# Kernel tuning notes

Measured on AMD Instinct MI355X. Metric: run time of the kernel, lower is better.

## Reference

```python
import jax, jax.numpy as jnp
import numpy as np

N_HEADS = 16
LN_EPS = 1e-5


def setup_inputs() -> dict:
    key = jax.random.key(0)
    ks = jax.random.split(key, 7)
    B, N, DIN, DCOND, NF = 2, 512, 1024, 128, 8
    return {
        "x": jax.random.normal(ks[0], (B, N, DIN), jnp.float32),
        "code": jax.random.normal(ks[1], (DCOND, NF), jnp.float32),
        "w_c": jax.random.normal(ks[2], (DIN, DCOND), jnp.float32) * 0.02,
        "W": jax.random.normal(ks[3], (3 * DIN, DIN), jnp.float32) * 0.02,
        "b": jax.random.normal(ks[4], (3 * DIN,), jnp.float32) * 0.02,
        "gamma": jnp.ones((DIN,), jnp.float32),
        "beta": jnp.zeros((DIN,), jnp.float32),
    }


def _layernorm(h, gamma, beta):
    mu = jnp.mean(h, axis=-1, keepdims=True)
    var = jnp.var(h, axis=-1, keepdims=True)
    return (h - mu) * jax.lax.rsqrt(var + LN_EPS) * gamma + beta


def reference(x, code, w_c, W, b, gamma, beta):
    B, N, din = x.shape
    nf = code.shape[1]
    H = N_HEADS
    hd = din // H
    scale = hd ** (-0.5)

    # ModLin2D: condition codes -> (nf, din), layernormed
    cond = _layernorm((w_c @ code).T, gamma, beta)            # (nf, din)
    # FiLM-style broadcasted multiply: (B, nf, N, din)
    modx = x[:, None, :, :] * cond[None, :, None, :]
    # projection to qkv: (B, nf, N, 3*din)
    qkv = jnp.einsum('bfnd,ed->bfne', modx, W) + b

    # split channel dim as (3, H, hd); torch view(3,H,hd,B,nf,N) on
    # channel-first layout == reshape (..., 3, H, hd) here
    qkv = qkv.reshape(B, nf, N, 3, H, hd)
    qkv = jnp.transpose(qkv, (3, 0, 4, 1, 2, 5))              # (3, B, H, nf, N, hd)
    q, k = qkv[0], qkv[1]

    scores = jnp.einsum('bhfnd,bhfmd->bhfnm', q, k) * scale   # (B, H, nf, N, N)
    attn = jax.nn.softmax(scores, axis=-1)
    # original torch code returns attn.size(); we return attn (the computed tensor)
    return attn
```

## Files before the change

kernel.cpp:

```cpp
#include <hip/hip_runtime.h>
#include <hip/hip_bf16.h>
#include <math.h>

#define NB    2
#define NSEQ  512
#define DIN   1024
#define DCOND 128
#define NF    8
#define NH    16
#define HD    64
constexpr float LN_EPS = 1e-5f;

#define WS_COND 0
#define WS_AHI  32768
#define WS_ALO  16809984
#define WS_BHI  33587200
#define WS_BLO  37781504
#define WS_QB   41975808
#define WS_KB   75530240

using bf16x8 = __attribute__((ext_vector_type(8))) short;
using f32x4  = __attribute__((ext_vector_type(4))) float;

__device__ __forceinline__ unsigned short f2bf(float x) {
    unsigned int u = __float_as_uint(x);
    unsigned int r = (u + 0x7fffu + ((u >> 16) & 1u)) >> 16;
    return (unsigned short)r;
}
__device__ __forceinline__ float bf2f(unsigned short h) {
    return __uint_as_float(((unsigned int)h) << 16);
}

__device__ __forceinline__ void gload16(const void* g, void* l) {
    __builtin_amdgcn_global_load_lds(
        (__attribute__((address_space(1))) void*)(const_cast<void*>(g)),
        (__attribute__((address_space(3))) void*)l, 16, 0, 0);
}

struct BF2 { bf16x8 hi, lo; };
__device__ __forceinline__ BF2 split8(float4 a, float4 b) {
    float v[8] = {a.x, a.y, a.z, a.w, b.x, b.y, b.z, b.w};
    BF2 r;
#pragma unroll
    for (int i = 0; i < 8; ++i) {
        unsigned u  = __float_as_uint(v[i]);
        unsigned uh = u & 0xffff0000u;
        r.hi[i] = (short)(u >> 16);
        float l = v[i] - __uint_as_float(uh);
        r.lo[i] = (short)(__float_as_uint(l) >> 16);
    }
    return r;
}

__global__ __launch_bounds__(256)
void cond_kernel(const float* __restrict__ w_c, const float* __restrict__ code,
                 const float* __restrict__ gamma, const float* __restrict__ beta,
                 float* __restrict__ cond)
{
    __shared__ float sc[DCOND];
    __shared__ float rs[256], rs2[256];
    const int f = blockIdx.x;
    const int t = threadIdx.x;

    if (t < DCOND) sc[t] = code[t * NF + f];
    __syncthreads();

    float hv[4];
    float s = 0.f, s2 = 0.f;
#pragma unroll
    for (int r = 0; r < 4; ++r) {
        const int d = r * 256 + t;
        const float* row = w_c + (size_t)d * DCOND;
        float acc = 0.f;
#pragma unroll 8
        for (int c = 0; c < DCOND; c += 4) {
            float4 wv = *(const float4*)(row + c);
            float4 cv = *(const float4*)(sc + c);
            acc += wv.x * cv.x + wv.y * cv.y + wv.z * cv.z + wv.w * cv.w;
        }
        hv[r] = acc; s += acc; s2 += acc * acc;
    }
    rs[t] = s; rs2[t] = s2;
    __syncthreads();
    for (int off = 128; off > 0; off >>= 1) {
        if (t < off) { rs[t] += rs[t + off]; rs2[t] += rs2[t + off]; }
        __syncthreads();
    }
    const float mu  = rs[0] * (1.f / DIN);
    const float var = rs2[0] * (1.f / DIN) - mu * mu;
    const float rstd = rsqrtf(var + LN_EPS);
#pragma unroll
    for (int r = 0; r < 4; ++r) {
        const int d = r * 256 + t;
        cond[f * DIN + d] = (hv[r] - mu) * rstd * gamma[d] + beta[d];
    }
}

__global__ __launch_bounds__(256)
void split_x_kernel(const float* __restrict__ x, const float* __restrict__ cond,
                    short* __restrict__ Ahi, short* __restrict__ Alo)
{
    const unsigned idx = blockIdx.x * 256 + threadIdx.x;
    const int d  = (idx & 127) * 8;
    const int n  = (idx >> 7) & 511;
    const int bf = idx >> 16;
    const int b  = bf >> 3, f = bf & 7;

    const float* xs = x + ((size_t)b * NSEQ + n) * DIN + d;
    const float* cs = cond + f * DIN + d;
    float4 x0 = *(const float4*)xs, x1 = *(const float4*)(xs + 4);
    float4 c0 = *(const float4*)cs, c1 = *(const float4*)(cs + 4);

    float m[8] = { x0.x*c0.x, x0.y*c0.y, x0.z*c0.z, x0.w*c0.w,
                   x1.x*c1.x, x1.y*c1.y, x1.z*c1.z, x1.w*c1.w };
    bf16x8 hi, lo;
#pragma unroll
    for (int i = 0; i < 8; ++i) {
        unsigned short h = f2bf(m[i]);
        hi[i] = (short)h;
        lo[i] = (short)f2bf(m[i] - bf2f(h));
    }
    *(bf16x8*)(Ahi + (size_t)idx * 8) = hi;
    *(bf16x8*)(Alo + (size_t)idx * 8) = lo;
}

__global__ __launch_bounds__(256)
void split_w_kernel(const float* __restrict__ W,
                    short* __restrict__ Bhi, short* __restrict__ Blo)
{
    const unsigned idx = blockIdx.x * 256 + threadIdx.x;
    const float* ws = W + (size_t)idx * 8;
    float4 w0 = *(const float4*)ws, w1 = *(const float4*)(ws + 4);
    float m[8] = { w0.x, w0.y, w0.z, w0.w, w1.x, w1.y, w1.z, w1.w };
    bf16x8 hi, lo;
#pragma unroll
    for (int i = 0; i < 8; ++i) {
        unsigned short h = f2bf(m[i]);
        hi[i] = (short)h;
        lo[i] = (short)f2bf(m[i] - bf2f(h));
    }
    *(bf16x8*)(Bhi + (size_t)idx * 8) = hi;
    *(bf16x8*)(Blo + (size_t)idx * 8) = lo;
}

__global__ __launch_bounds__(256, 2)
void proj_mfma_kernel(const short* __restrict__ Ahi_g, const short* __restrict__ Alo_g,
                      const short* __restrict__ Bhi_g, const short* __restrict__ Blo_g,
                      const float* __restrict__ bias,
                      float* __restrict__ Qb, float* __restrict__ Kb)
{
    __shared__ short sAhi[128 * 32];
    __shared__ short sAlo[128 * 32];
    __shared__ short sBhi[128 * 32];
    __shared__ short sBlo[128 * 32];

    const int bf   = blockIdx.z;
    const int n0   = blockIdx.y * 128;
    const int bcol = blockIdx.x * 128;
    const int t    = threadIdx.x;
    const int w    = t >> 6, lane = t & 63;
    const int wr   = w >> 1, wc = w & 1;

    const int rl = lane >> 2;
    const int sl = (lane & 3) ^ ((lane >> 3) & 3);
    const size_t aoff = ((size_t)bf * NSEQ + n0 + 32 * w + rl) * DIN + sl * 8;
    const size_t boff = ((size_t)(bcol + 32 * w + rl)) * DIN + sl * 8;
    const short* gAh = Ahi_g + aoff;
    const short* gAl = Alo_g + aoff;
    const short* gBh = Bhi_g + boff;
    const short* gBl = Blo_g + boff;
    short* dAh = sAhi + 1024 * w;
    short* dAl = sAlo + 1024 * w;
    short* dBh = sBhi + 1024 * w;
    short* dBl = sBlo + 1024 * w;

    int offA[4], offB[4];
    const int g = lane >> 4;
#pragma unroll
    for (int fi = 0; fi < 4; ++fi) {
        int r  = wr * 64 + fi * 16 + (lane & 15);
        offA[fi] = r * 32 + ((g ^ ((r >> 1) & 3)) * 8);
        int rb = wc * 64 + fi * 16 + (lane & 15);
        offB[fi] = rb * 32 + ((g ^ ((rb >> 1) & 3)) * 8);
    }

    f32x4 acc[4][4];
#pragma unroll
    for (int i = 0; i < 4; ++i)
#pragma unroll
        for (int j = 0; j < 4; ++j) acc[i][j] = (f32x4){0.f, 0.f, 0.f, 0.f};

    for (int kb = 0; kb < DIN; kb += 32) {
        __syncthreads();
        gload16(gAh + kb, dAh);  gload16(gAh + kb + 16 * DIN, dAh + 512);
        gload16(gAl + kb, dAl);  gload16(gAl + kb + 16 * DIN, dAl + 512);
        gload16(gBh + kb, dBh);  gload16(gBh + kb + 16 * DIN, dBh + 512);
        gload16(gBl + kb, dBl);  gload16(gBl + kb + 16 * DIN, dBl + 512);
        __syncthreads();

        bf16x8 Ah[4], Al[4], Bh[4], Bl[4];
#pragma unroll
        for (int fi = 0; fi < 4; ++fi) {
            Ah[fi] = *(const bf16x8*)(sAhi + offA[fi]);
            Al[fi] = *(const bf16x8*)(sAlo + offA[fi]);
            Bh[fi] = *(const bf16x8*)(sBhi + offB[fi]);
            Bl[fi] = *(const bf16x8*)(sBlo + offB[fi]);
        }
#pragma unroll
        for (int i = 0; i < 4; ++i)
#pragma unroll
            for (int j = 0; j < 4; ++j) {
                acc[i][j] = __builtin_amdgcn_mfma_f32_16x16x32_bf16(Ah[i], Bh[j], acc[i][j], 0, 0, 0);
                acc[i][j] = __builtin_amdgcn_mfma_f32_16x16x32_bf16(Ah[i], Bl[j], acc[i][j], 0, 0, 0);
                acc[i][j] = __builtin_amdgcn_mfma_f32_16x16x32_bf16(Al[i], Bh[j], acc[i][j], 0, 0, 0);
            }
    }

#pragma unroll
    for (int j = 0; j < 4; ++j) {
        const int e = bcol + wc * 64 + j * 16 + (lane & 15);
        const float bv = bias[e];
        const int ek = e & 1023;
        float* dst = ((e < DIN) ? Qb : Kb)
                   + ((size_t)(bf * NH + (ek >> 6)) * NSEQ) * HD + (ek & 63);
#pragma unroll
        for (int i = 0; i < 4; ++i) {
            const int rbase = n0 + wr * 64 + i * 16 + (lane >> 4) * 4;
            f32x4 v = acc[i][j];
#pragma unroll
            for (int rg = 0; rg < 4; ++rg)
                dst[(size_t)(rbase + rg) * HD] = v[rg] + bv;
        }
    }
}

__global__ __launch_bounds__(256, 2)
void scores_mfma_kernel(const float* __restrict__ Qb, const float* __restrict__ Kb,
                        float* __restrict__ out)
{
    __shared__ float Kl_lds[128 * 64];

    const int bfh = blockIdx.y;
    const int rt  = blockIdx.x;
    const int t = threadIdx.x, w = t >> 6, lane = t & 63;
    const int g = lane >> 4, c16 = lane & 15;

    const float* Qp = Qb + ((size_t)bfh * NSEQ + rt * 64 + 16 * w + c16) * HD;
    BF2 qf[2];
#pragma unroll
    for (int ks = 0; ks < 2; ++ks) {
        float4 a = *(const float4*)(Qp + 32 * ks + 8 * g);
        float4 b = *(const float4*)(Qp + 32 * ks + 8 * g + 4);
        qf[ks] = split8(a, b);
    }

    const float* Kp = Kb + (size_t)bfh * NSEQ * HD;
    const int swz = (lane & 7) << 4;

    f32x4 acc[32];
#pragma unroll
    for (int i = 0; i < 32; ++i) acc[i] = (f32x4){0.f, 0.f, 0.f, 0.f};

#pragma unroll
    for (int c = 0; c < 4; ++c) {
        __syncthreads();
#pragma unroll
        for (int i = 0; i < 8; ++i) {
            const int row = 32 * w + 4 * i + g;
            const int slot = c16 ^ (row & 7);
            gload16(Kp + ((size_t)(c * 128 + row)) * HD + slot * 4,
                    Kl_lds + (32 * w + 4 * i) * HD);
        }
        __syncthreads();

#pragma unroll
        for (int mtl = 0; mtl < 8; ++mtl) {
            const int row = 16 * mtl + c16;
            const char* rbase = (const char*)Kl_lds + row * 256;
#pragma unroll
            for (int ks = 0; ks < 2; ++ks) {
                const int o = 128 * ks + 32 * g;
                float4 a = *(const float4*)(rbase + ((o)      ^ swz));
                float4 b = *(const float4*)(rbase + ((o + 16) ^ swz));
                BF2 kf = split8(a, b);
                f32x4 d = acc[c * 8 + mtl];
                d = __builtin_amdgcn_mfma_f32_16x16x32_bf16(kf.hi, qf[ks].hi, d, 0, 0, 0);
                d = __builtin_amdgcn_mfma_f32_16x16x32_bf16(kf.hi, qf[ks].lo, d, 0, 0, 0);
                d = __builtin_amdgcn_mfma_f32_16x16x32_bf16(kf.lo, qf[ks].hi, d, 0, 0, 0);
                acc[c * 8 + mtl] = d;
            }
        }
    }

    float m = -1e30f;
#pragma unroll
    for (int i = 0; i < 32; ++i)
#pragma unroll
        for (int r = 0; r < 4; ++r) m = fmaxf(m, acc[i][r]);
    m = fmaxf(m, __shfl_xor(m, 16));
    m = fmaxf(m, __shfl_xor(m, 32));

    float s = 0.f;
#pragma unroll
    for (int i = 0; i < 32; ++i)
#pragma unroll
        for (int r = 0; r < 4; ++r) {
            float e = __expf((acc[i][r] - m) * 0.125f);
            acc[i][r] = e;
            s += e;
        }
    s += __shfl_xor(s, 16);
    s += __shfl_xor(s, 32);
    const float inv = 1.f / s;

    const int b = bfh >> 7, f = (bfh >> 4) & 7, h = bfh & 15;
    const int n = rt * 64 + 16 * w + c16;
    float* rowp = out + ((((size_t)(b * NH + h)) * NF + f) * NSEQ + n) * NSEQ;
#pragma unroll
    for (int i = 0; i < 32; ++i) {
        f32x4 v = acc[i] * inv;
        *(f32x4*)(rowp + 16 * i + 4 * g) = v;
    }
}

extern "C" void kernel_launch(void* const* d_in, const int* in_sizes, int n_in,
                              void* d_out, int out_size, void* d_ws, size_t ws_size,
                              hipStream_t stream)
{
    const float* x     = (const float*)d_in[0];
    const float* code  = (const float*)d_in[1];
    const float* w_c   = (const float*)d_in[2];
    const float* W     = (const float*)d_in[3];
    const float* bias  = (const float*)d_in[4];
    const float* gamma = (const float*)d_in[5];
    const float* beta  = (const float*)d_in[6];
    float* out = (float*)d_out;

    char* ws = (char*)d_ws;
    float* cond = (float*)(ws + WS_COND);
    short* Ahi  = (short*)(ws + WS_AHI);
    short* Alo  = (short*)(ws + WS_ALO);
    short* Bhi  = (short*)(ws + WS_BHI);
    short* Blo  = (short*)(ws + WS_BLO);
    float* Qb   = (float*)(ws + WS_QB);
    float* Kb   = (float*)(ws + WS_KB);

    cond_kernel<<<NF, 256, 0, stream>>>(w_c, code, gamma, beta, cond);
    split_x_kernel<<<4096, 256, 0, stream>>>(x, cond, Ahi, Alo);
    split_w_kernel<<<1024, 256, 0, stream>>>(W, Bhi, Blo);

    dim3 gP(16, 4, NB * NF);
    proj_mfma_kernel<<<gP, 256, 0, stream>>>(Ahi, Alo, Bhi, Blo, bias, Qb, Kb);

    dim3 gS(8, NB * NF * NH);
    scores_mfma_kernel<<<gS, 256, 0, stream>>>(Qb, Kb, out);
}
```

Baseline: 469.7 us.

## Emit pre-split bf16 Q/K from projection and double-buffer K tiles in scores

The projection epilogue now writes Q and K as bf16 hi/lo pairs, so the scores kernel no longer reruns the float-to-bf16 split on every K tile it reads. The scores kernel double-buffers K tiles in LDS with a new swizzle, loading the next chunk while MFMAs run on the current one. split_x now loads cond into LDS once and loops over all 8 filters per x element, reading x once instead of eight times. The costs are a larger LDS footprint in scores, which may lower occupancy, and more scattered 2-byte stores in the projection epilogue.

```diff
diff --git a/kernel.cpp b/kernel.cpp
--- a/kernel.cpp
+++ b/kernel.cpp
@@ -16,8 +16,10 @@
 #define WS_ALO  16809984
 #define WS_BHI  33587200
 #define WS_BLO  37781504
-#define WS_QB   41975808
-#define WS_KB   75530240
+#define WS_QH   41975808
+#define WS_QL   58753024
+#define WS_KH   75530240
+#define WS_KL   92307456
 
 using bf16x8 = __attribute__((ext_vector_type(8))) short;
 using f32x4  = __attribute__((ext_vector_type(4))) float;
@@ -35,21 +37,6 @@
     __builtin_amdgcn_global_load_lds(
         (__attribute__((address_space(1))) void*)(const_cast<void*>(g)),
         (__attribute__((address_space(3))) void*)l, 16, 0, 0);
-}
-
-struct BF2 { bf16x8 hi, lo; };
-__device__ __forceinline__ BF2 split8(float4 a, float4 b) {
-    float v[8] = {a.x, a.y, a.z, a.w, b.x, b.y, b.z, b.w};
-    BF2 r;
-#pragma unroll
-    for (int i = 0; i < 8; ++i) {
-        unsigned u  = __float_as_uint(v[i]);
-        unsigned uh = u & 0xffff0000u;
-        r.hi[i] = (short)(u >> 16);
-        float l = v[i] - __uint_as_float(uh);
-        r.lo[i] = (short)(__float_as_uint(l) >> 16);
-    }
-    return r;
 }
 
 __global__ __launch_bounds__(256)
@@ -100,28 +87,39 @@
 void split_x_kernel(const float* __restrict__ x, const float* __restrict__ cond,
                     short* __restrict__ Ahi, short* __restrict__ Alo)
 {
-    const unsigned idx = blockIdx.x * 256 + threadIdx.x;
-    const int d  = (idx & 127) * 8;
-    const int n  = (idx >> 7) & 511;
-    const int bf = idx >> 16;
-    const int b  = bf >> 3, f = bf & 7;
-
-    const float* xs = x + ((size_t)b * NSEQ + n) * DIN + d;
-    const float* cs = cond + f * DIN + d;
+    __shared__ float sc[NF * DIN];
+    const int t = threadIdx.x;
+#pragma unroll
+    for (int i = 0; i < 8; ++i)
+        *(float4*)(sc + i * 1024 + t * 4) = *(const float4*)(cond + i * 1024 + t * 4);
+    __syncthreads();
+
+    const unsigned gid = blockIdx.x * 256 + t;
+    const int dg = gid & 127;
+    const int n  = (gid >> 7) & 511;
+    const int b  = gid >> 16;
+
+    const float* xs = x + ((size_t)b * NSEQ + n) * DIN + dg * 8;
     float4 x0 = *(const float4*)xs, x1 = *(const float4*)(xs + 4);
-    float4 c0 = *(const float4*)cs, c1 = *(const float4*)(cs + 4);
-
-    float m[8] = { x0.x*c0.x, x0.y*c0.y, x0.z*c0.z, x0.w*c0.w,
-                   x1.x*c1.x, x1.y*c1.y, x1.z*c1.z, x1.w*c1.w };
-    bf16x8 hi, lo;
-#pragma unroll
-    for (int i = 0; i < 8; ++i) {
-        unsigned short h = f2bf(m[i]);
-        hi[i] = (short)h;
-        lo[i] = (short)f2bf(m[i] - bf2f(h));
-    }
-    *(bf16x8*)(Ahi + (size_t)idx * 8) = hi;
-    *(bf16x8*)(Alo + (size_t)idx * 8) = lo;
+    float xv[8] = {x0.x, x0.y, x0.z, x0.w, x1.x, x1.y, x1.z, x1.w};
+
+#pragma unroll
+    for (int f = 0; f < 8; ++f) {
+        const float* cs = sc + f * DIN + dg * 8;
+        float4 c0 = *(const float4*)cs, c1 = *(const float4*)(cs + 4);
+        float cv[8] = {c0.x, c0.y, c0.z, c0.w, c1.x, c1.y, c1.z, c1.w};
+        bf16x8 hi, lo;
+#pragma unroll
+        for (int i = 0; i < 8; ++i) {
+            float m = xv[i] * cv[i];
+            unsigned short h = f2bf(m);
+            hi[i] = (short)h;
+            lo[i] = (short)f2bf(m - bf2f(h));
+        }
+        const size_t off = (size_t)(b * 8 + f) * 524288 + n * 1024 + dg * 8;
+        *(bf16x8*)(Ahi + off) = hi;
+        *(bf16x8*)(Alo + off) = lo;
+    }
 }
 
 __global__ __launch_bounds__(256)
@@ -147,7 +145,8 @@
 void proj_mfma_kernel(const short* __restrict__ Ahi_g, const short* __restrict__ Alo_g,
                       const short* __restrict__ Bhi_g, const short* __restrict__ Blo_g,
                       const float* __restrict__ bias,
-                      float* __restrict__ Qb, float* __restrict__ Kb)
+                      short* __restrict__ Qh, short* __restrict__ Ql,
+                      short* __restrict__ Kh, short* __restrict__ Kl)
 {
     __shared__ short sAhi[128 * 32];
     __shared__ short sAlo[128 * 32];
@@ -221,76 +220,93 @@
         const int e = bcol + wc * 64 + j * 16 + (lane & 15);
         const float bv = bias[e];
         const int ek = e & 1023;
-        float* dst = ((e < DIN) ? Qb : Kb)
-                   + ((size_t)(bf * NH + (ek >> 6)) * NSEQ) * HD + (ek & 63);
+        const size_t base = ((size_t)(bf * NH + (ek >> 6)) * NSEQ) * HD + (ek & 63);
+        short* dh = ((e < DIN) ? Qh : Kh) + base;
+        short* dl = ((e < DIN) ? Ql : Kl) + base;
 #pragma unroll
         for (int i = 0; i < 4; ++i) {
             const int rbase = n0 + wr * 64 + i * 16 + (lane >> 4) * 4;
             f32x4 v = acc[i][j];
 #pragma unroll
-            for (int rg = 0; rg < 4; ++rg)
-                dst[(size_t)(rbase + rg) * HD] = v[rg] + bv;
+            for (int rg = 0; rg < 4; ++rg) {
+                const float u = v[rg] + bv;
+                const unsigned uu = __float_as_uint(u);
+                const float lo = u - __uint_as_float(uu & 0xffff0000u);
+                dh[(size_t)(rbase + rg) * HD] = (short)(uu >> 16);
+                dl[(size_t)(rbase + rg) * HD] = (short)(__float_as_uint(lo) >> 16);
+            }
         }
     }
 }
 
 __global__ __launch_bounds__(256, 2)
-void scores_mfma_kernel(const float* __restrict__ Qb, const float* __restrict__ Kb,
+void scores_mfma_kernel(const short* __restrict__ Qh, const short* __restrict__ Ql,
+                        const short* __restrict__ Kh, const short* __restrict__ Kl,
                         float* __restrict__ out)
 {
-    __shared__ float Kl_lds[128 * 64];
+    __shared__ short KhL[2][128 * 64];
+    __shared__ short KlL[2][128 * 64];
 
     const int bfh = blockIdx.y;
     const int rt  = blockIdx.x;
     const int t = threadIdx.x, w = t >> 6, lane = t & 63;
     const int g = lane >> 4, c16 = lane & 15;
 
-    const float* Qp = Qb + ((size_t)bfh * NSEQ + rt * 64 + 16 * w + c16) * HD;
-    BF2 qf[2];
+    const size_t qoff = ((size_t)bfh * NSEQ + rt * 64 + 16 * w + c16) * HD;
+    bf16x8 qh[2], ql[2];
 #pragma unroll
     for (int ks = 0; ks < 2; ++ks) {
-        float4 a = *(const float4*)(Qp + 32 * ks + 8 * g);
-        float4 b = *(const float4*)(Qp + 32 * ks + 8 * g + 4);
-        qf[ks] = split8(a, b);
-    }
-
-    const float* Kp = Kb + (size_t)bfh * NSEQ * HD;
-    const int swz = (lane & 7) << 4;
+        qh[ks] = *(const bf16x8*)(Qh + qoff + ks * 32 + 8 * g);
+        ql[ks] = *(const bf16x8*)(Ql + qoff + ks * 32 + 8 * g);
+    }
+
+    const short* Khg = Kh + (size_t)bfh * NSEQ * HD;
+    const short* Klg = Kl + (size_t)bfh * NSEQ * HD;
+    const int sr    = lane >> 3;
+    const int sslot = (lane & 7) ^ sr;
+    const int rsw   = c16 & 7;
 
     f32x4 acc[32];
 #pragma unroll
     for (int i = 0; i < 32; ++i) acc[i] = (f32x4){0.f, 0.f, 0.f, 0.f};
 
+#define STAGE(s, c)                                                            \
+    _Pragma("unroll")                                                          \
+    for (int i = 0; i < 4; ++i) {                                              \
+        const int r0 = 32 * w + 8 * i;                                         \
+        gload16(Khg + ((size_t)((c) * 128 + r0 + sr)) * HD + sslot * 8,        \
+                &KhL[s][r0 * 64]);                                             \
+        gload16(Klg + ((size_t)((c) * 128 + r0 + sr)) * HD + sslot * 8,        \
+                &KlL[s][r0 * 64]);                                             \
+    }
+
+    STAGE(0, 0)
+    __syncthreads();
+
 #pragma unroll
     for (int c = 0; c < 4; ++c) {
-        __syncthreads();
-#pragma unroll
-        for (int i = 0; i < 8; ++i) {
-            const int row = 32 * w + 4 * i + g;
-            const int slot = c16 ^ (row & 7);
-            gload16(Kp + ((size_t)(c * 128 + row)) * HD + slot * 4,
-                    Kl_lds + (32 * w + 4 * i) * HD);
-        }
-        __syncthreads();
+        if (c < 3) STAGE((c + 1) & 1, c + 1)
 
 #pragma unroll
         for (int mtl = 0; mtl < 8; ++mtl) {
             const int row = 16 * mtl + c16;
-            const char* rbase = (const char*)Kl_lds + row * 256;
+            const short* bh = &KhL[c & 1][row * 64];
+            const short* bl = &KlL[c & 1][row * 64];
+            f32x4 d = acc[c * 8 + mtl];
 #pragma unroll
             for (int ks = 0; ks < 2; ++ks) {
-                const int o = 128 * ks + 32 * g;
-                float4 a = *(const float4*)(rbase + ((o)      ^ swz));
-                float4 b = *(const float4*)(rbase + ((o + 16) ^ swz));
-                BF2 kf = split8(a, b);
-                f32x4 d = acc[c * 8 + mtl];
-                d = __builtin_amdgcn_mfma_f32_16x16x32_bf16(kf.hi, qf[ks].hi, d, 0, 0, 0);
-                d = __builtin_amdgcn_mfma_f32_16x16x32_bf16(kf.hi, qf[ks].lo, d, 0, 0, 0);
-                d = __builtin_amdgcn_mfma_f32_16x16x32_bf16(kf.lo, qf[ks].hi, d, 0, 0, 0);
-                acc[c * 8 + mtl] = d;
+                const int so = ((ks * 4 + g) ^ rsw) * 8;
+                bf16x8 ah = *(const bf16x8*)(bh + so);
+                bf16x8 al = *(const bf16x8*)(bl + so);
+                d = __builtin_amdgcn_mfma_f32_16x16x32_bf16(ah, qh[ks], d, 0, 0, 0);
+                d = __builtin_amdgcn_mfma_f32_16x16x32_bf16(ah, ql[ks], d, 0, 0, 0);
+                d = __builtin_amdgcn_mfma_f32_16x16x32_bf16(al, qh[ks], d, 0, 0, 0);
             }
-        }
-    }
+            acc[c * 8 + mtl] = d;
+        }
+        __syncthreads();
+    }
+#undef STAGE
 
     float m = -1e30f;
 #pragma unroll
@@ -342,16 +358,18 @@
     short* Alo  = (short*)(ws + WS_ALO);
     short* Bhi  = (short*)(ws + WS_BHI);
     short* Blo  = (short*)(ws + WS_BLO);
-    float* Qb   = (float*)(ws + WS_QB);
-    float* Kb   = (float*)(ws + WS_KB);
+    short* Qh   = (short*)(ws + WS_QH);
+    short* Ql   = (short*)(ws + WS_QL);
+    short* Kh   = (short*)(ws + WS_KH);
+    short* Kl   = (short*)(ws + WS_KL);
 
     cond_kernel<<<NF, 256, 0, stream>>>(w_c, code, gamma, beta, cond);
-    split_x_kernel<<<4096, 256, 0, stream>>>(x, cond, Ahi, Alo);
+    split_x_kernel<<<512, 256, 0, stream>>>(x, cond, Ahi, Alo);
     split_w_kernel<<<1024, 256, 0, stream>>>(W, Bhi, Blo);
 
     dim3 gP(16, 4, NB * NF);
-    proj_mfma_kernel<<<gP, 256, 0, stream>>>(Ahi, Alo, Bhi, Blo, bias, Qb, Kb);
+    proj_mfma_kernel<<<gP, 256, 0, stream>>>(Ahi, Alo, Bhi, Blo, bias, Qh, Ql, Kh, Kl);
 
     dim3 gS(8, NB * NF * NH);
-    scores_mfma_kernel<<<gS, 256, 0, stream>>>(Qb, Kb, out);
-}
+    scores_mfma_kernel<<<gS, 256, 0, stream>>>(Qh, Ql, Kh, Kl, out);
+}
```

Result: slower. 493.0 us (+4.9%).
